# Kernel optimization log

Hardware: AMD Instinct MI355X
Metric: run time of the kernel (lower is better)

Reference implementation:

```python
import jax, jax.numpy as jnp
import numpy as np

DATA_BITS = 108
SHIFT_BITS = 7


def setup_inputs() -> dict:
    key = jax.random.key(0)
    kx, ks = jax.random.split(key)
    B = 1_000_000
    X = jax.random.randint(kx, (B, DATA_BITS), 0, 2).astype(jnp.float32)
    shift = jax.random.randint(ks, (B, SHIFT_BITS), 0, 2).astype(jnp.int32)
    return {"X": X, "shift": shift}


def reference(X, shift):
    # 7-stage barrel left shift (toward lower indices, MSB-first layout).
    # VecMUX(s, a, b) = s*a + (1-s)*b with s in {0,1}.
    current = X
    s_f = shift.astype(X.dtype)  # [B, 7]
    for layer in range(SHIFT_BITS):
        shift_amt = 2 ** (SHIFT_BITS - 1 - layer)
        if shift_amt >= DATA_BITS:
            shifted = jnp.zeros_like(current)
        else:
            shifted = jnp.concatenate(
                [current[..., shift_amt:], jnp.zeros_like(current[..., :shift_amt])],
                axis=-1,
            )
        s = s_f[..., layer:layer + 1]  # [B, 1]
        current = s * shifted + (1.0 - s) * current
    return current
```

## Files before the change

kernel.cpp:

```cpp
#include <hip/hip_runtime.h>

#define DATA_BITS 108
#define SHIFT_BITS 7
#define F4_PER_ROW 27
#define ROWS_PER_TILE 256

typedef float f32x4 __attribute__((ext_vector_type(4)));

__global__ __launch_bounds__(ROWS_PER_TILE) void barrel_fused_kernel(
    const float* __restrict__ X,
    const int* __restrict__ shift,
    float* __restrict__ out, int rows) {
    __shared__ int sS[ROWS_PER_TILE];

    const int row0 = blockIdx.x * ROWS_PER_TILE;
    const int t = threadIdx.x;
    const int N = rows * DATA_BITS;

    const int r = row0 + t;
    if (r < rows) {
        const int* p = shift + r * SHIFT_BITS;
        int s = 0;
        #pragma unroll
        for (int l = 0; l < SHIFT_BITS; ++l) s = (s << 1) | (p[l] & 1);
        sS[t] = s;
    }
    __syncthreads();

    const int nrows = min(ROWS_PER_TILE, rows - row0);
    const int units = nrows * F4_PER_ROW;
    for (int u = t; u < units; u += ROWS_PER_TILE) {
        const int rb = u / F4_PER_ROW;
        const int q  = u - rb * F4_PER_ROW;
        const int s  = sS[rb];
        const int valid = DATA_BITS - s;
        const int i0 = q * 4;

        f32x4 rv = {0.f, 0.f, 0.f, 0.f};
        if (i0 < valid) {
            const int s_al = s & ~3;
            const int m    = s & 3;
            const int idx_lo = (row0 + rb) * DATA_BITS + i0 + s_al;
            int idx_hi = idx_lo + 4;
            idx_hi = min(idx_hi, N - 4);
            const f32x4 lo = *reinterpret_cast<const f32x4*>(X + idx_lo);
            const f32x4 hi = *reinterpret_cast<const f32x4*>(X + idx_hi);

            const bool m2 = (m & 2) != 0;
            const bool m1 = (m & 1) != 0;
            const float t0 = m2 ? lo[2] : lo[0];
            const float t1 = m2 ? lo[3] : lo[1];
            const float t2 = m2 ? hi[0] : lo[2];
            const float t3 = m2 ? hi[1] : lo[3];
            const float t4 = m2 ? hi[2] : hi[0];
            rv[0] = m1 ? t1 : t0;
            rv[1] = m1 ? t2 : t1;
            rv[2] = m1 ? t3 : t2;
            rv[3] = m1 ? t4 : t3;

            rv[0] = (i0 + 0 < valid) ? rv[0] : 0.f;
            rv[1] = (i0 + 1 < valid) ? rv[1] : 0.f;
            rv[2] = (i0 + 2 < valid) ? rv[2] : 0.f;
            rv[3] = (i0 + 3 < valid) ? rv[3] : 0.f;
        }
        f32x4* dst = reinterpret_cast<f32x4*>(out + (long long)(row0 + rb) * DATA_BITS + i0);
        __builtin_nontemporal_store(rv, dst);
    }
}

extern "C" void kernel_launch(void* const* d_in, const int* in_sizes, int n_in,
                              void* d_out, int out_size, void* d_ws, size_t ws_size,
                              hipStream_t stream) {
    const float* X     = (const float*)d_in[0];
    const int*   shift = (const int*)d_in[1];
    float*       out   = (float*)d_out;

    const int rows = in_sizes[1] / SHIFT_BITS;
    const int grid = (rows + ROWS_PER_TILE - 1) / ROWS_PER_TILE;

    barrel_fused_kernel<<<grid, ROWS_PER_TILE, 0, stream>>>(X, shift, out, rows);
}
```

Baseline: 141.3 us.

## Coalesce shift loads via shared memory and unroll full-tile loop branch-free

```diff
diff --git a/kernel.cpp b/kernel.cpp
--- a/kernel.cpp
+++ b/kernel.cpp
@@ -3,68 +3,100 @@
 #define DATA_BITS 108
 #define SHIFT_BITS 7
 #define F4_PER_ROW 27
-#define ROWS_PER_TILE 256
+#define RPT 256
 
 typedef float f32x4 __attribute__((ext_vector_type(4)));
+typedef int   i32x4 __attribute__((ext_vector_type(4)));
 
-__global__ __launch_bounds__(ROWS_PER_TILE) void barrel_fused_kernel(
+__global__ __launch_bounds__(RPT) void barrel_fused_kernel(
     const float* __restrict__ X,
     const int* __restrict__ shift,
     float* __restrict__ out, int rows) {
-    __shared__ int sS[ROWS_PER_TILE];
 
-    const int row0 = blockIdx.x * ROWS_PER_TILE;
+    __shared__ int sRaw[RPT * SHIFT_BITS];
+    __shared__ int sS[RPT];
+
+    const int row0 = blockIdx.x * RPT;
     const int t = threadIdx.x;
     const int N = rows * DATA_BITS;
 
-    const int r = row0 + t;
-    if (r < rows) {
-        const int* p = shift + r * SHIFT_BITS;
+    const int total_sh = rows * SHIFT_BITS;
+    const int base_sh  = row0 * SHIFT_BITS;
+    #pragma unroll
+    for (int kk = 0; kk < 2; ++kk) {
+        const int li = (t + kk * RPT) * 4;
+        if (li < RPT * SHIFT_BITS) {
+            const int gi = base_sh + li;
+            if (gi + 4 <= total_sh) {
+                *reinterpret_cast<i32x4*>(&sRaw[li]) =
+                    *reinterpret_cast<const i32x4*>(&shift[gi]);
+            } else {
+                #pragma unroll
+                for (int j = 0; j < 4; ++j)
+                    sRaw[li + j] = (gi + j < total_sh) ? shift[gi + j] : 0;
+            }
+        }
+    }
+    __syncthreads();
+
+    {
         int s = 0;
         #pragma unroll
-        for (int l = 0; l < SHIFT_BITS; ++l) s = (s << 1) | (p[l] & 1);
+        for (int l = 0; l < SHIFT_BITS; ++l) s = (s << 1) | (sRaw[t * SHIFT_BITS + l] & 1);
         sS[t] = s;
     }
     __syncthreads();
 
-    const int nrows = min(ROWS_PER_TILE, rows - row0);
-    const int units = nrows * F4_PER_ROW;
-    for (int u = t; u < units; u += ROWS_PER_TILE) {
-        const int rb = u / F4_PER_ROW;
-        const int q  = u - rb * F4_PER_ROW;
-        const int s  = sS[rb];
+    auto process = [&](int rb, int q) {
+        const int s     = sS[rb];
         const int valid = DATA_BITS - s;
-        const int i0 = q * 4;
+        const int i0    = q * 4;
+        const int i0e   = min(i0, max(valid - 1, 0) & ~3);
+        const int rowbase = (row0 + rb) * DATA_BITS;
+        int idx_lo = rowbase + i0e + (s & ~3);
+        idx_lo = min(idx_lo, N - 4);
+        const int idx_hi = min(idx_lo + 4, N - 4);
+        const f32x4 lo = *reinterpret_cast<const f32x4*>(X + idx_lo);
+        const f32x4 hi = *reinterpret_cast<const f32x4*>(X + idx_hi);
+        const int  m  = s & 3;
+        const bool m2 = (m & 2) != 0;
+        const bool m1 = (m & 1) != 0;
+        const float t0 = m2 ? lo[2] : lo[0];
+        const float t1 = m2 ? lo[3] : lo[1];
+        const float t2 = m2 ? hi[0] : lo[2];
+        const float t3 = m2 ? hi[1] : lo[3];
+        const float t4 = m2 ? hi[2] : hi[0];
+        f32x4 rv;
+        rv[0] = m1 ? t1 : t0;
+        rv[1] = m1 ? t2 : t1;
+        rv[2] = m1 ? t3 : t2;
+        rv[3] = m1 ? t4 : t3;
+        rv[0] = (i0 + 0 < valid) ? rv[0] : 0.f;
+        rv[1] = (i0 + 1 < valid) ? rv[1] : 0.f;
+        rv[2] = (i0 + 2 < valid) ? rv[2] : 0.f;
+        rv[3] = (i0 + 3 < valid) ? rv[3] : 0.f;
+        __builtin_nontemporal_store(rv,
+            reinterpret_cast<f32x4*>(out + rowbase + i0));
+    };
 
-        f32x4 rv = {0.f, 0.f, 0.f, 0.f};
-        if (i0 < valid) {
-            const int s_al = s & ~3;
-            const int m    = s & 3;
-            const int idx_lo = (row0 + rb) * DATA_BITS + i0 + s_al;
-            int idx_hi = idx_lo + 4;
-            idx_hi = min(idx_hi, N - 4);
-            const f32x4 lo = *reinterpret_cast<const f32x4*>(X + idx_lo);
-            const f32x4 hi = *reinterpret_cast<const f32x4*>(X + idx_hi);
-
-            const bool m2 = (m & 2) != 0;
-            const bool m1 = (m & 1) != 0;
-            const float t0 = m2 ? lo[2] : lo[0];
-            const float t1 = m2 ? lo[3] : lo[1];
-            const float t2 = m2 ? hi[0] : lo[2];
-            const float t3 = m2 ? hi[1] : lo[3];
-            const float t4 = m2 ? hi[2] : hi[0];
-            rv[0] = m1 ? t1 : t0;
-            rv[1] = m1 ? t2 : t1;
-            rv[2] = m1 ? t3 : t2;
-            rv[3] = m1 ? t4 : t3;
-
-            rv[0] = (i0 + 0 < valid) ? rv[0] : 0.f;
-            rv[1] = (i0 + 1 < valid) ? rv[1] : 0.f;
-            rv[2] = (i0 + 2 < valid) ? rv[2] : 0.f;
-            rv[3] = (i0 + 3 < valid) ? rv[3] : 0.f;
+    const int nrows = min(RPT, rows - row0);
+    if (nrows == RPT) {
+        int rb = t / F4_PER_ROW;
+        int q  = t - rb * F4_PER_ROW;
+        #pragma unroll 9
+        for (int k = 0; k < F4_PER_ROW; ++k) {
+            process(rb, q);
+            q  += 13;
+            rb += 9;
+            if (q >= F4_PER_ROW) { q -= F4_PER_ROW; rb += 1; }
         }
-        f32x4* dst = reinterpret_cast<f32x4*>(out + (long long)(row0 + rb) * DATA_BITS + i0);
-        __builtin_nontemporal_store(rv, dst);
+    } else {
+        const int units = nrows * F4_PER_ROW;
+        for (int u = t; u < units; u += RPT) {
+            const int rb = u / F4_PER_ROW;
+            const int q  = u - rb * F4_PER_ROW;
+            process(rb, q);
+        }
     }
 }
 
@@ -76,7 +108,7 @@
     float*       out   = (float*)d_out;
 
     const int rows = in_sizes[1] / SHIFT_BITS;
-    const int grid = (rows + ROWS_PER_TILE - 1) / ROWS_PER_TILE;
+    const int grid = (rows + RPT - 1) / RPT;
 
-    barrel_fused_kernel<<<grid, ROWS_PER_TILE, 0, stream>>>(X, shift, out, rows);
+    barrel_fused_kernel<<<grid, RPT, 0, stream>>>(X, shift, out, rows);
 }
```

Result: slower. 149.5 us (+5.8%).
